# Kernel tuning notes

Measured on AMD Instinct MI355X. Metric: run time of the kernel, lower is better.

Reference implementation:

```python
import jax, jax.numpy as jnp
import numpy as np

T = 48        # target_size
B = 128       # batch of sequences (vmapped version of the per-sequence module)
S = 512       # seq_len
START = 46    # start_index
END = 47      # end_index
MIN = 0.0001  # self.minimum


def setup_inputs() -> dict:
    key = jax.random.key(0)
    k1, k2 = jax.random.split(key)
    features = jax.random.normal(k1, (B, S, T), dtype=jnp.float32)
    # __init_transition__: uniform matrix with start column / end row zeroed,
    # then MIN placed at those zeroed positions.
    u = jax.random.uniform(k2, (T, T), dtype=jnp.float32)
    start_mask = 1.0 - jax.nn.one_hot(jnp.full((T,), START), T)          # zeros column START
    end_mask = 1.0 - jax.nn.one_hot(jnp.full((T,), END), T).T            # zeros row END
    value = (1.0 - start_mask * end_mask) * MIN                          # MIN where masked out
    transition = u * start_mask * end_mask + value
    return {"features": features, "transition": transition}


def reference(features, transition):
    # CRF forward (partition-function) score, faithful to forward_score(),
    # batched over B sequences. features: [B, S, T], transition: [T, T].
    fv0 = MIN * (1.0 - jax.nn.one_hot(START, T, dtype=jnp.float32))      # [T]
    fv0 = jnp.broadcast_to(fv0, (B, T))

    def step(fv, feat_t):
        # score[b, i, j] = fv[b, j] + transition[i, j] + feat_t[b, i]
        score = fv[:, None, :] + transition[None, :, :] + feat_t[:, :, None]  # [B, T, T]
        # Faithful replication of the source's log_sum_exp: the max subtracted
        # inside exp is the per-row max indexed by j (column position), while the
        # max added back is indexed by i.
        rowmax = jnp.max(score, axis=2)                                   # [B, T]
        new_fv = rowmax + jnp.log(jnp.sum(jnp.exp(score - rowmax[:, None, :]), axis=2))
        return new_fv, None

    feats_time_major = jnp.swapaxes(features, 0, 1)                       # [S, B, T]
    fv, _ = jax.lax.scan(step, fv0, feats_time_major)

    # Terminal transition to END, then a single-row logsumexp (standard here).
    sc = fv + transition[END][None, :]                                    # [B, T]
    m = jnp.max(sc, axis=1)                                               # [B]
    return m + jnp.log(jnp.sum(jnp.exp(sc - m[:, None]), axis=1))         # [B]
```

## Files before the change

### kernel.cpp

```cpp
#include <hip/hip_runtime.h>
#include <math.h>


#define TT 48
#define BB 128
#define SS 512
#define STARTI 46
#define ENDI 47
#define MINV 0.0001f
#define CHUNK 32
#define NCHUNK (SS / CHUNK)
#define GPT 6
#define LOG2E 1.44269504088896340736f
#define LN2   0.69314718055994530942f

#if __has_builtin(__builtin_amdgcn_exp2f)
#define EXP2F(x) __builtin_amdgcn_exp2f(x)
#else
#define EXP2F(x) exp2f(x)
#endif
#if __has_builtin(__builtin_amdgcn_logf)
#define LOG2F(x) __builtin_amdgcn_logf(x)
#else
#define LOG2F(x) log2f(x)
#endif

template <int CTRL>
__device__ __forceinline__ float qperm_f(float x) {
#if __has_builtin(__builtin_amdgcn_update_dpp)
    return __int_as_float(__builtin_amdgcn_update_dpp(
        0, __float_as_int(x), CTRL, 0xF, 0xF, true));
#elif __has_builtin(__builtin_amdgcn_mov_dpp)
    return __int_as_float(
        __builtin_amdgcn_mov_dpp(__float_as_int(x), CTRL, 0xF, 0xF, true));
#else
    return __shfl_xor(x, (CTRL == 0xB1) ? 1 : 2, 64);
#endif
}

#if __has_builtin(__builtin_amdgcn_global_load_lds)
#define HAVE_GLOAD 1
__device__ __forceinline__ void gload16(const float* g, float* l) {
    __builtin_amdgcn_global_load_lds(
        (const __attribute__((address_space(1))) void*)g,
        (__attribute__((address_space(3))) void*)l, 16, 0, 0);
}
#else
#define HAVE_GLOAD 0
#endif

__global__ __launch_bounds__(64, 1) void crf_forward_kernel(
    const float* __restrict__ feats,
    const float* __restrict__ trans,
    float* __restrict__ out)
{
    const int lane = threadIdx.x;
    const int i16  = lane >> 2;
    const int jsub = lane & 3;
    const int j0   = jsub * 12;
    const int b    = blockIdx.x;

    __shared__ __align__(16) float fvb[TT];
    __shared__ __align__(16) float hb[TT];
    __shared__ __align__(16) float featbuf[2][CHUNK * TT];

    float tr2[3][12], E[3][12];
#pragma unroll
    for (int r = 0; r < 3; ++r) {
#pragma unroll
        for (int q = 0; q < 3; ++q) {
            float4 v = *reinterpret_cast<const float4*>(
                trans + (i16 + 16 * r) * TT + j0 + 4 * q);
            tr2[r][4 * q + 0] = v.x * LOG2E; tr2[r][4 * q + 1] = v.y * LOG2E;
            tr2[r][4 * q + 2] = v.z * LOG2E; tr2[r][4 * q + 3] = v.w * LOG2E;
        }
#pragma unroll
        for (int q = 0; q < 12; ++q) E[r][q] = EXP2F(tr2[r][q]);
    }

    const float* fb = feats + (size_t)b * SS * TT;

#if HAVE_GLOAD
#pragma unroll
    for (int k = 0; k < GPT; ++k)
        gload16(fb + k * 256 + lane * 4, &featbuf[0][k * 256]);
#else
#pragma unroll
    for (int k = 0; k < GPT; ++k)
        *reinterpret_cast<float4*>(&featbuf[0][k * 256 + lane * 4]) =
            *reinterpret_cast<const float4*>(fb + k * 256 + lane * 4);
#endif

    if (lane < TT) fvb[lane] = (lane == STARTI) ? 0.0f : (MINV * LOG2E);
    float fvi[3];
#pragma unroll
    for (int r = 0; r < 3; ++r)
        fvi[r] = ((i16 + 16 * r) == STARTI) ? 0.0f : (MINV * LOG2E);

#if HAVE_GLOAD
    asm volatile("s_waitcnt vmcnt(0)" ::: "memory");
#endif

    for (int c = 0; c < NCHUNK; ++c) {
        const int buf = c & 1;
        const bool hp = (c + 1 < NCHUNK);
        if (hp) {
#if HAVE_GLOAD
#pragma unroll
            for (int k = 0; k < GPT; ++k)
                gload16(fb + (c + 1) * (CHUNK * TT) + k * 256 + lane * 4,
                        &featbuf[buf ^ 1][k * 256]);
#else
#pragma unroll
            for (int k = 0; k < GPT; ++k)
                *reinterpret_cast<float4*>(&featbuf[buf ^ 1][k * 256 + lane * 4]) =
                    *reinterpret_cast<const float4*>(
                        fb + (c + 1) * (CHUNK * TT) + k * 256 + lane * 4);
#endif
        }

        for (int sl = 0; sl < CHUNK; ++sl) {
            float feat2[3];
#pragma unroll
            for (int r = 0; r < 3; ++r)
                feat2[r] = featbuf[buf][sl * TT + i16 + 16 * r] * LOG2E;

            float4 v0 = *reinterpret_cast<const float4*>(&fvb[j0]);
            float4 v1 = *reinterpret_cast<const float4*>(&fvb[j0 + 4]);
            float4 v2 = *reinterpret_cast<const float4*>(&fvb[j0 + 8]);
            float fvs[12] = {v0.x, v0.y, v0.z, v0.w, v1.x, v1.y,
                             v1.z, v1.w, v2.x, v2.y, v2.z, v2.w};

            float hs[3], qv2[3];
#pragma unroll
            for (int r = 0; r < 3; ++r) {
                float a[12];
#pragma unroll
                for (int q = 0; q < 12; ++q) a[q] = fvs[q] + tr2[r][q];
                float m0 = fmaxf(fmaxf(a[0], a[1]),  a[2]);
                float m1 = fmaxf(fmaxf(a[3], a[4]),  a[5]);
                float m2 = fmaxf(fmaxf(a[6], a[7]),  a[8]);
                float m3 = fmaxf(fmaxf(a[9], a[10]), a[11]);
                float M2 = fmaxf(fmaxf(fmaxf(m0, m1), m2), m3);
                M2 = fmaxf(M2, qperm_f<0xB1>(M2));
                M2 = fmaxf(M2, qperm_f<0x4E>(M2));
                hs[r]  = EXP2F((fvi[r] - feat2[r]) - M2);
                qv2[r] = M2 + 2.0f * feat2[r];
            }
            if (jsub == 0) {
                hb[i16]      = hs[0];
                hb[i16 + 16] = hs[1];
                hb[i16 + 32] = hs[2];
            }
            float4 h0 = *reinterpret_cast<const float4*>(&hb[j0]);
            float4 h1 = *reinterpret_cast<const float4*>(&hb[j0 + 4]);
            float4 h2 = *reinterpret_cast<const float4*>(&hb[j0 + 8]);
            float hv[12] = {h0.x, h0.y, h0.z, h0.w, h1.x, h1.y,
                            h1.z, h1.w, h2.x, h2.y, h2.z, h2.w};

            float nfv[3];
#pragma unroll
            for (int r = 0; r < 3; ++r) {
                float d0 = E[r][0] * hv[0], d1 = E[r][1] * hv[1];
                float d2 = E[r][2] * hv[2], d3 = E[r][3] * hv[3];
                d0 = fmaf(E[r][4],  hv[4],  d0); d1 = fmaf(E[r][5],  hv[5],  d1);
                d2 = fmaf(E[r][6],  hv[6],  d2); d3 = fmaf(E[r][7],  hv[7],  d3);
                d0 = fmaf(E[r][8],  hv[8],  d0); d1 = fmaf(E[r][9],  hv[9],  d1);
                d2 = fmaf(E[r][10], hv[10], d2); d3 = fmaf(E[r][11], hv[11], d3);
                float dot = (d0 + d1) + (d2 + d3);
                dot += qperm_f<0xB1>(dot);
                dot += qperm_f<0x4E>(dot);
                nfv[r] = qv2[r] + LOG2F(dot);
                fvi[r] = nfv[r];
            }
            if (jsub == 0) {
                fvb[i16]      = nfv[0];
                fvb[i16 + 16] = nfv[1];
                fvb[i16 + 32] = nfv[2];
            }
#if HAVE_GLOAD
            if (sl == CHUNK - 2 && hp)
                asm volatile("s_waitcnt vmcnt(0)" ::: "memory");
#endif
        }
    }

    {
        const float* te = trans + ENDI * TT;
        float sc[TT];
#pragma unroll
        for (int q = 0; q < 12; ++q) {
            float4 fv4 = *reinterpret_cast<const float4*>(&fvb[4 * q]);
            float4 te4 = *reinterpret_cast<const float4*>(te + 4 * q);
            sc[4 * q + 0] = fmaf(fv4.x, LN2, te4.x);
            sc[4 * q + 1] = fmaf(fv4.y, LN2, te4.y);
            sc[4 * q + 2] = fmaf(fv4.z, LN2, te4.z);
            sc[4 * q + 3] = fmaf(fv4.w, LN2, te4.w);
        }
        float m = sc[0];
#pragma unroll
        for (int j = 1; j < TT; ++j) m = fmaxf(m, sc[j]);
        float s = 0.0f;
#pragma unroll
        for (int j = 0; j < TT; ++j) s += __expf(sc[j] - m);
        if (lane == 0) out[b] = m + __logf(s);
    }
}

extern "C" void kernel_launch(void* const* d_in, const int* in_sizes, int n_in,
                              void* d_out, int out_size, void* d_ws, size_t ws_size,
                              hipStream_t stream) {
    (void)in_sizes; (void)n_in; (void)out_size; (void)d_ws; (void)ws_size;
    const float* feats = (const float*)d_in[0];
    const float* trans = (const float*)d_in[1];
    float* out = (float*)d_out;
    crf_forward_kernel<<<dim3(BB), dim3(64), 0, stream>>>(feats, trans, out);
}
```

Before: 258.2 us.

## Interleave two independent sequences per wavefront to hide serial-step latency

```diff
diff --git a/kernel.cpp b/kernel.cpp
--- a/kernel.cpp
+++ b/kernel.cpp
@@ -8,6 +8,8 @@
 #define STARTI 46
 #define ENDI 47
 #define MINV 0.0001f
+#define KSEQ 2
+#define NBLK (BB / KSEQ)
 #define CHUNK 32
 #define NCHUNK (SS / CHUNK)
 #define GPT 6
@@ -58,11 +60,11 @@
     const int i16  = lane >> 2;
     const int jsub = lane & 3;
     const int j0   = jsub * 12;
-    const int b    = blockIdx.x;
-
-    __shared__ __align__(16) float fvb[TT];
-    __shared__ __align__(16) float hb[TT];
-    __shared__ __align__(16) float featbuf[2][CHUNK * TT];
+    const int b0   = blockIdx.x * KSEQ;
+
+    __shared__ __align__(16) float fvb[KSEQ][TT];
+    __shared__ __align__(16) float hb[KSEQ][TT];
+    __shared__ __align__(16) float featbuf[KSEQ][2][CHUNK * TT];
 
     float tr2[3][12], E[3][12];
 #pragma unroll
@@ -78,24 +80,36 @@
         for (int q = 0; q < 12; ++q) E[r][q] = EXP2F(tr2[r][q]);
     }
 
-    const float* fb = feats + (size_t)b * SS * TT;
-
-#if HAVE_GLOAD
-#pragma unroll
-    for (int k = 0; k < GPT; ++k)
-        gload16(fb + k * 256 + lane * 4, &featbuf[0][k * 256]);
-#else
-#pragma unroll
-    for (int k = 0; k < GPT; ++k)
-        *reinterpret_cast<float4*>(&featbuf[0][k * 256 + lane * 4]) =
-            *reinterpret_cast<const float4*>(fb + k * 256 + lane * 4);
-#endif
-
-    if (lane < TT) fvb[lane] = (lane == STARTI) ? 0.0f : (MINV * LOG2E);
-    float fvi[3];
-#pragma unroll
-    for (int r = 0; r < 3; ++r)
-        fvi[r] = ((i16 + 16 * r) == STARTI) ? 0.0f : (MINV * LOG2E);
+    const float* fbs[KSEQ];
+#pragma unroll
+    for (int s = 0; s < KSEQ; ++s)
+        fbs[s] = feats + (size_t)(b0 + s) * SS * TT;
+
+#pragma unroll
+    for (int s = 0; s < KSEQ; ++s) {
+#if HAVE_GLOAD
+#pragma unroll
+        for (int k = 0; k < GPT; ++k)
+            gload16(fbs[s] + k * 256 + lane * 4, &featbuf[s][0][k * 256]);
+#else
+#pragma unroll
+        for (int k = 0; k < GPT; ++k)
+            *reinterpret_cast<float4*>(&featbuf[s][0][k * 256 + lane * 4]) =
+                *reinterpret_cast<const float4*>(fbs[s] + k * 256 + lane * 4);
+#endif
+    }
+
+    if (lane < TT) {
+#pragma unroll
+        for (int s = 0; s < KSEQ; ++s)
+            fvb[s][lane] = (lane == STARTI) ? 0.0f : (MINV * LOG2E);
+    }
+    float fvi[KSEQ][3];
+#pragma unroll
+    for (int s = 0; s < KSEQ; ++s)
+#pragma unroll
+        for (int r = 0; r < 3; ++r)
+            fvi[s][r] = ((i16 + 16 * r) == STARTI) ? 0.0f : (MINV * LOG2E);
 
 #if HAVE_GLOAD
     asm volatile("s_waitcnt vmcnt(0)" ::: "memory");
@@ -105,78 +119,111 @@
         const int buf = c & 1;
         const bool hp = (c + 1 < NCHUNK);
         if (hp) {
-#if HAVE_GLOAD
-#pragma unroll
-            for (int k = 0; k < GPT; ++k)
-                gload16(fb + (c + 1) * (CHUNK * TT) + k * 256 + lane * 4,
-                        &featbuf[buf ^ 1][k * 256]);
-#else
-#pragma unroll
-            for (int k = 0; k < GPT; ++k)
-                *reinterpret_cast<float4*>(&featbuf[buf ^ 1][k * 256 + lane * 4]) =
-                    *reinterpret_cast<const float4*>(
-                        fb + (c + 1) * (CHUNK * TT) + k * 256 + lane * 4);
-#endif
+#pragma unroll
+            for (int s = 0; s < KSEQ; ++s) {
+#if HAVE_GLOAD
+#pragma unroll
+                for (int k = 0; k < GPT; ++k)
+                    gload16(fbs[s] + (c + 1) * (CHUNK * TT) + k * 256 + lane * 4,
+                            &featbuf[s][buf ^ 1][k * 256]);
+#else
+#pragma unroll
+                for (int k = 0; k < GPT; ++k)
+                    *reinterpret_cast<float4*>(
+                        &featbuf[s][buf ^ 1][k * 256 + lane * 4]) =
+                        *reinterpret_cast<const float4*>(
+                            fbs[s] + (c + 1) * (CHUNK * TT) + k * 256 + lane * 4);
+#endif
+            }
         }
 
         for (int sl = 0; sl < CHUNK; ++sl) {
-            float feat2[3];
-#pragma unroll
-            for (int r = 0; r < 3; ++r)
-                feat2[r] = featbuf[buf][sl * TT + i16 + 16 * r] * LOG2E;
-
-            float4 v0 = *reinterpret_cast<const float4*>(&fvb[j0]);
-            float4 v1 = *reinterpret_cast<const float4*>(&fvb[j0 + 4]);
-            float4 v2 = *reinterpret_cast<const float4*>(&fvb[j0 + 8]);
-            float fvs[12] = {v0.x, v0.y, v0.z, v0.w, v1.x, v1.y,
-                             v1.z, v1.w, v2.x, v2.y, v2.z, v2.w};
-
-            float hs[3], qv2[3];
-#pragma unroll
-            for (int r = 0; r < 3; ++r) {
-                float a[12];
-#pragma unroll
-                for (int q = 0; q < 12; ++q) a[q] = fvs[q] + tr2[r][q];
-                float m0 = fmaxf(fmaxf(a[0], a[1]),  a[2]);
-                float m1 = fmaxf(fmaxf(a[3], a[4]),  a[5]);
-                float m2 = fmaxf(fmaxf(a[6], a[7]),  a[8]);
-                float m3 = fmaxf(fmaxf(a[9], a[10]), a[11]);
-                float M2 = fmaxf(fmaxf(fmaxf(m0, m1), m2), m3);
-                M2 = fmaxf(M2, qperm_f<0xB1>(M2));
-                M2 = fmaxf(M2, qperm_f<0x4E>(M2));
-                hs[r]  = EXP2F((fvi[r] - feat2[r]) - M2);
-                qv2[r] = M2 + 2.0f * feat2[r];
+            float feat2[KSEQ][3];
+#pragma unroll
+            for (int s = 0; s < KSEQ; ++s)
+#pragma unroll
+                for (int r = 0; r < 3; ++r)
+                    feat2[s][r] =
+                        featbuf[s][buf][sl * TT + i16 + 16 * r] * LOG2E;
+
+            float fvs[KSEQ][12];
+#pragma unroll
+            for (int s = 0; s < KSEQ; ++s) {
+                float4 v0 = *reinterpret_cast<const float4*>(&fvb[s][j0]);
+                float4 v1 = *reinterpret_cast<const float4*>(&fvb[s][j0 + 4]);
+                float4 v2 = *reinterpret_cast<const float4*>(&fvb[s][j0 + 8]);
+                fvs[s][0] = v0.x; fvs[s][1] = v0.y; fvs[s][2]  = v0.z; fvs[s][3]  = v0.w;
+                fvs[s][4] = v1.x; fvs[s][5] = v1.y; fvs[s][6]  = v1.z; fvs[s][7]  = v1.w;
+                fvs[s][8] = v2.x; fvs[s][9] = v2.y; fvs[s][10] = v2.z; fvs[s][11] = v2.w;
+            }
+
+            float hs[KSEQ][3], qv2[KSEQ][3];
+#pragma unroll
+            for (int s = 0; s < KSEQ; ++s) {
+#pragma unroll
+                for (int r = 0; r < 3; ++r) {
+                    float a[12];
+#pragma unroll
+                    for (int q = 0; q < 12; ++q) a[q] = fvs[s][q] + tr2[r][q];
+                    float m0 = fmaxf(fmaxf(a[0], a[1]),  a[2]);
+                    float m1 = fmaxf(fmaxf(a[3], a[4]),  a[5]);
+                    float m2 = fmaxf(fmaxf(a[6], a[7]),  a[8]);
+                    float m3 = fmaxf(fmaxf(a[9], a[10]), a[11]);
+                    float M2 = fmaxf(fmaxf(fmaxf(m0, m1), m2), m3);
+                    M2 = fmaxf(M2, qperm_f<0xB1>(M2));
+                    M2 = fmaxf(M2, qperm_f<0x4E>(M2));
+                    hs[s][r]  = EXP2F((fvi[s][r] - feat2[s][r]) - M2);
+                    qv2[s][r] = M2 + 2.0f * feat2[s][r];
+                }
             }
             if (jsub == 0) {
-                hb[i16]      = hs[0];
-                hb[i16 + 16] = hs[1];
-                hb[i16 + 32] = hs[2];
-            }
-            float4 h0 = *reinterpret_cast<const float4*>(&hb[j0]);
-            float4 h1 = *reinterpret_cast<const float4*>(&hb[j0 + 4]);
-            float4 h2 = *reinterpret_cast<const float4*>(&hb[j0 + 8]);
-            float hv[12] = {h0.x, h0.y, h0.z, h0.w, h1.x, h1.y,
-                            h1.z, h1.w, h2.x, h2.y, h2.z, h2.w};
-
-            float nfv[3];
-#pragma unroll
-            for (int r = 0; r < 3; ++r) {
-                float d0 = E[r][0] * hv[0], d1 = E[r][1] * hv[1];
-                float d2 = E[r][2] * hv[2], d3 = E[r][3] * hv[3];
-                d0 = fmaf(E[r][4],  hv[4],  d0); d1 = fmaf(E[r][5],  hv[5],  d1);
-                d2 = fmaf(E[r][6],  hv[6],  d2); d3 = fmaf(E[r][7],  hv[7],  d3);
-                d0 = fmaf(E[r][8],  hv[8],  d0); d1 = fmaf(E[r][9],  hv[9],  d1);
-                d2 = fmaf(E[r][10], hv[10], d2); d3 = fmaf(E[r][11], hv[11], d3);
-                float dot = (d0 + d1) + (d2 + d3);
-                dot += qperm_f<0xB1>(dot);
-                dot += qperm_f<0x4E>(dot);
-                nfv[r] = qv2[r] + LOG2F(dot);
-                fvi[r] = nfv[r];
+#pragma unroll
+                for (int s = 0; s < KSEQ; ++s) {
+                    hb[s][i16]      = hs[s][0];
+                    hb[s][i16 + 16] = hs[s][1];
+                    hb[s][i16 + 32] = hs[s][2];
+                }
+            }
+            float hv[KSEQ][12];
+#pragma unroll
+            for (int s = 0; s < KSEQ; ++s) {
+                float4 h0 = *reinterpret_cast<const float4*>(&hb[s][j0]);
+                float4 h1 = *reinterpret_cast<const float4*>(&hb[s][j0 + 4]);
+                float4 h2 = *reinterpret_cast<const float4*>(&hb[s][j0 + 8]);
+                hv[s][0] = h0.x; hv[s][1] = h0.y; hv[s][2]  = h0.z; hv[s][3]  = h0.w;
+                hv[s][4] = h1.x; hv[s][5] = h1.y; hv[s][6]  = h1.z; hv[s][7]  = h1.w;
+                hv[s][8] = h2.x; hv[s][9] = h2.y; hv[s][10] = h2.z; hv[s][11] = h2.w;
+            }
+
+            float nfv[KSEQ][3];
+#pragma unroll
+            for (int s = 0; s < KSEQ; ++s) {
+#pragma unroll
+                for (int r = 0; r < 3; ++r) {
+                    float d0 = E[r][0] * hv[s][0], d1 = E[r][1] * hv[s][1];
+                    float d2 = E[r][2] * hv[s][2], d3 = E[r][3] * hv[s][3];
+                    d0 = fmaf(E[r][4],  hv[s][4],  d0);
+                    d1 = fmaf(E[r][5],  hv[s][5],  d1);
+                    d2 = fmaf(E[r][6],  hv[s][6],  d2);
+                    d3 = fmaf(E[r][7],  hv[s][7],  d3);
+                    d0 = fmaf(E[r][8],  hv[s][8],  d0);
+                    d1 = fmaf(E[r][9],  hv[s][9],  d1);
+                    d2 = fmaf(E[r][10], hv[s][10], d2);
+                    d3 = fmaf(E[r][11], hv[s][11], d3);
+                    float dot = (d0 + d1) + (d2 + d3);
+                    dot += qperm_f<0xB1>(dot);
+                    dot += qperm_f<0x4E>(dot);
+                    nfv[s][r] = qv2[s][r] + LOG2F(dot);
+                    fvi[s][r] = nfv[s][r];
+                }
             }
             if (jsub == 0) {
-                fvb[i16]      = nfv[0];
-                fvb[i16 + 16] = nfv[1];
-                fvb[i16 + 32] = nfv[2];
+#pragma unroll
+                for (int s = 0; s < KSEQ; ++s) {
+                    fvb[s][i16]      = nfv[s][0];
+                    fvb[s][i16 + 16] = nfv[s][1];
+                    fvb[s][i16 + 32] = nfv[s][2];
+                }
             }
 #if HAVE_GLOAD
             if (sl == CHUNK - 2 && hp)
@@ -187,23 +234,26 @@
 
     {
         const float* te = trans + ENDI * TT;
-        float sc[TT];
-#pragma unroll
-        for (int q = 0; q < 12; ++q) {
-            float4 fv4 = *reinterpret_cast<const float4*>(&fvb[4 * q]);
-            float4 te4 = *reinterpret_cast<const float4*>(te + 4 * q);
-            sc[4 * q + 0] = fmaf(fv4.x, LN2, te4.x);
-            sc[4 * q + 1] = fmaf(fv4.y, LN2, te4.y);
-            sc[4 * q + 2] = fmaf(fv4.z, LN2, te4.z);
-            sc[4 * q + 3] = fmaf(fv4.w, LN2, te4.w);
-        }
-        float m = sc[0];
-#pragma unroll
-        for (int j = 1; j < TT; ++j) m = fmaxf(m, sc[j]);
-        float s = 0.0f;
-#pragma unroll
-        for (int j = 0; j < TT; ++j) s += __expf(sc[j] - m);
-        if (lane == 0) out[b] = m + __logf(s);
+#pragma unroll
+        for (int s = 0; s < KSEQ; ++s) {
+            float sc[TT];
+#pragma unroll
+            for (int q = 0; q < 12; ++q) {
+                float4 fv4 = *reinterpret_cast<const float4*>(&fvb[s][4 * q]);
+                float4 te4 = *reinterpret_cast<const float4*>(te + 4 * q);
+                sc[4 * q + 0] = fmaf(fv4.x, LN2, te4.x);
+                sc[4 * q + 1] = fmaf(fv4.y, LN2, te4.y);
+                sc[4 * q + 2] = fmaf(fv4.z, LN2, te4.z);
+                sc[4 * q + 3] = fmaf(fv4.w, LN2, te4.w);
+            }
+            float m = sc[0];
+#pragma unroll
+            for (int j = 1; j < TT; ++j) m = fmaxf(m, sc[j]);
+            float sum = 0.0f;
+#pragma unroll
+            for (int j = 0; j < TT; ++j) sum += __expf(sc[j] - m);
+            if (lane == 0) out[b0 + s] = m + __logf(sum);
+        }
     }
 }
 
@@ -214,5 +264,5 @@
     const float* feats = (const float*)d_in[0];
     const float* trans = (const float*)d_in[1];
     float* out = (float*)d_out;
-    crf_forward_kernel<<<dim3(BB), dim3(64), 0, stream>>>(feats, trans, out);
-}
+    crf_forward_kernel<<<dim3(NBLK), dim3(64), 0, stream>>>(feats, trans, out);
+}
```

Measured after the change: 410.6 us. 1.59x slower.

## Assign one full row per lane instead of splitting rows across four lanes

Applied to the files above, without the earlier changes.

```diff
diff --git a/kernel.cpp b/kernel.cpp
--- a/kernel.cpp
+++ b/kernel.cpp
@@ -25,19 +25,6 @@
 #define LOG2F(x) log2f(x)
 #endif
 
-template <int CTRL>
-__device__ __forceinline__ float qperm_f(float x) {
-#if __has_builtin(__builtin_amdgcn_update_dpp)
-    return __int_as_float(__builtin_amdgcn_update_dpp(
-        0, __float_as_int(x), CTRL, 0xF, 0xF, true));
-#elif __has_builtin(__builtin_amdgcn_mov_dpp)
-    return __int_as_float(
-        __builtin_amdgcn_mov_dpp(__float_as_int(x), CTRL, 0xF, 0xF, true));
-#else
-    return __shfl_xor(x, (CTRL == 0xB1) ? 1 : 2, 64);
-#endif
-}
-
 #if __has_builtin(__builtin_amdgcn_global_load_lds)
 #define HAVE_GLOAD 1
 __device__ __forceinline__ void gload16(const float* g, float* l) {
@@ -49,34 +36,32 @@
 #define HAVE_GLOAD 0
 #endif
 
+__device__ __forceinline__ float m3(float a, float b, float c) {
+    return fmaxf(fmaxf(a, b), c);
+}
+
 __global__ __launch_bounds__(64, 1) void crf_forward_kernel(
     const float* __restrict__ feats,
     const float* __restrict__ trans,
     float* __restrict__ out)
 {
     const int lane = threadIdx.x;
-    const int i16  = lane >> 2;
-    const int jsub = lane & 3;
-    const int j0   = jsub * 12;
+    const int row  = (lane < TT) ? lane : TT - 1;
     const int b    = blockIdx.x;
 
-    __shared__ __align__(16) float fvb[TT];
-    __shared__ __align__(16) float hb[TT];
+    __shared__ __align__(16) float fvx[TT];
+    __shared__ __align__(16) float hx[TT];
     __shared__ __align__(16) float featbuf[2][CHUNK * TT];
 
-    float tr2[3][12], E[3][12];
+    float tr2r[TT], Er[TT];
 #pragma unroll
-    for (int r = 0; r < 3; ++r) {
+    for (int q = 0; q < 12; ++q) {
+        float4 v = *reinterpret_cast<const float4*>(trans + row * TT + 4 * q);
+        tr2r[4 * q + 0] = v.x * LOG2E; tr2r[4 * q + 1] = v.y * LOG2E;
+        tr2r[4 * q + 2] = v.z * LOG2E; tr2r[4 * q + 3] = v.w * LOG2E;
+    }
 #pragma unroll
-        for (int q = 0; q < 3; ++q) {
-            float4 v = *reinterpret_cast<const float4*>(
-                trans + (i16 + 16 * r) * TT + j0 + 4 * q);
-            tr2[r][4 * q + 0] = v.x * LOG2E; tr2[r][4 * q + 1] = v.y * LOG2E;
-            tr2[r][4 * q + 2] = v.z * LOG2E; tr2[r][4 * q + 3] = v.w * LOG2E;
-        }
-#pragma unroll
-        for (int q = 0; q < 12; ++q) E[r][q] = EXP2F(tr2[r][q]);
-    }
+    for (int k = 0; k < TT; ++k) Er[k] = EXP2F(tr2r[k]);
 
     const float* fb = feats + (size_t)b * SS * TT;
 
@@ -91,11 +76,8 @@
             *reinterpret_cast<const float4*>(fb + k * 256 + lane * 4);
 #endif
 
-    if (lane < TT) fvb[lane] = (lane == STARTI) ? 0.0f : (MINV * LOG2E);
-    float fvi[3];
-#pragma unroll
-    for (int r = 0; r < 3; ++r)
-        fvi[r] = ((i16 + 16 * r) == STARTI) ? 0.0f : (MINV * LOG2E);
+    if (lane < TT) fvx[lane] = (lane == STARTI) ? 0.0f : (MINV * LOG2E);
+    float fv2i = (row == STARTI) ? 0.0f : (MINV * LOG2E);
 
 #if HAVE_GLOAD
     asm volatile("s_waitcnt vmcnt(0)" ::: "memory");
@@ -120,64 +102,54 @@
         }
 
         for (int sl = 0; sl < CHUNK; ++sl) {
-            float feat2[3];
+            const float feat2 = featbuf[buf][sl * TT + row] * LOG2E;
+
+            float g[TT];
 #pragma unroll
-            for (int r = 0; r < 3; ++r)
-                feat2[r] = featbuf[buf][sl * TT + i16 + 16 * r] * LOG2E;
+            for (int q = 0; q < 12; ++q) {
+                float4 v = *reinterpret_cast<const float4*>(&fvx[4 * q]);
+                g[4 * q + 0] = v.x; g[4 * q + 1] = v.y;
+                g[4 * q + 2] = v.z; g[4 * q + 3] = v.w;
+            }
+            float a[TT];
+#pragma unroll
+            for (int k = 0; k < TT; ++k) a[k] = g[k] + tr2r[k];
+            float t16[16];
+#pragma unroll
+            for (int u = 0; u < 16; ++u)
+                t16[u] = m3(a[3 * u], a[3 * u + 1], a[3 * u + 2]);
+            float t6_0 = m3(t16[0],  t16[1],  t16[2]);
+            float t6_1 = m3(t16[3],  t16[4],  t16[5]);
+            float t6_2 = m3(t16[6],  t16[7],  t16[8]);
+            float t6_3 = m3(t16[9],  t16[10], t16[11]);
+            float t6_4 = m3(t16[12], t16[13], t16[14]);
+            float t6_5 = t16[15];
+            const float M2 = fmaxf(m3(t6_0, t6_1, t6_2), m3(t6_3, t6_4, t6_5));
 
-            float4 v0 = *reinterpret_cast<const float4*>(&fvb[j0]);
-            float4 v1 = *reinterpret_cast<const float4*>(&fvb[j0 + 4]);
-            float4 v2 = *reinterpret_cast<const float4*>(&fvb[j0 + 8]);
-            float fvs[12] = {v0.x, v0.y, v0.z, v0.w, v1.x, v1.y,
-                             v1.z, v1.w, v2.x, v2.y, v2.z, v2.w};
+            const float h   = EXP2F((fv2i - feat2) - M2);
+            const float qv2 = M2 + 2.0f * feat2;
+            if (lane < TT) hx[lane] = h;
 
-            float hs[3], qv2[3];
+            float hg[TT];
 #pragma unroll
-            for (int r = 0; r < 3; ++r) {
-                float a[12];
+            for (int q = 0; q < 12; ++q) {
+                float4 v = *reinterpret_cast<const float4*>(&hx[4 * q]);
+                hg[4 * q + 0] = v.x; hg[4 * q + 1] = v.y;
+                hg[4 * q + 2] = v.z; hg[4 * q + 3] = v.w;
+            }
+            float acc[8];
 #pragma unroll
-                for (int q = 0; q < 12; ++q) a[q] = fvs[q] + tr2[r][q];
-                float m0 = fmaxf(fmaxf(a[0], a[1]),  a[2]);
-                float m1 = fmaxf(fmaxf(a[3], a[4]),  a[5]);
-                float m2 = fmaxf(fmaxf(a[6], a[7]),  a[8]);
-                float m3 = fmaxf(fmaxf(a[9], a[10]), a[11]);
-                float M2 = fmaxf(fmaxf(fmaxf(m0, m1), m2), m3);
-                M2 = fmaxf(M2, qperm_f<0xB1>(M2));
-                M2 = fmaxf(M2, qperm_f<0x4E>(M2));
-                hs[r]  = EXP2F((fvi[r] - feat2[r]) - M2);
-                qv2[r] = M2 + 2.0f * feat2[r];
-            }
-            if (jsub == 0) {
-                hb[i16]      = hs[0];
-                hb[i16 + 16] = hs[1];
-                hb[i16 + 32] = hs[2];
-            }
-            float4 h0 = *reinterpret_cast<const float4*>(&hb[j0]);
-            float4 h1 = *reinterpret_cast<const float4*>(&hb[j0 + 4]);
-            float4 h2 = *reinterpret_cast<const float4*>(&hb[j0 + 8]);
-            float hv[12] = {h0.x, h0.y, h0.z, h0.w, h1.x, h1.y,
-                            h1.z, h1.w, h2.x, h2.y, h2.z, h2.w};
+            for (int u = 0; u < 8; ++u) acc[u] = Er[u] * hg[u];
+#pragma unroll
+            for (int k = 8; k < TT; ++k)
+                acc[k & 7] = fmaf(Er[k], hg[k], acc[k & 7]);
+            const float dot = ((acc[0] + acc[1]) + (acc[2] + acc[3]))
+                            + ((acc[4] + acc[5]) + (acc[6] + acc[7]));
 
-            float nfv[3];
-#pragma unroll
-            for (int r = 0; r < 3; ++r) {
-                float d0 = E[r][0] * hv[0], d1 = E[r][1] * hv[1];
-                float d2 = E[r][2] * hv[2], d3 = E[r][3] * hv[3];
-                d0 = fmaf(E[r][4],  hv[4],  d0); d1 = fmaf(E[r][5],  hv[5],  d1);
-                d2 = fmaf(E[r][6],  hv[6],  d2); d3 = fmaf(E[r][7],  hv[7],  d3);
-                d0 = fmaf(E[r][8],  hv[8],  d0); d1 = fmaf(E[r][9],  hv[9],  d1);
-                d2 = fmaf(E[r][10], hv[10], d2); d3 = fmaf(E[r][11], hv[11], d3);
-                float dot = (d0 + d1) + (d2 + d3);
-                dot += qperm_f<0xB1>(dot);
-                dot += qperm_f<0x4E>(dot);
-                nfv[r] = qv2[r] + LOG2F(dot);
-                fvi[r] = nfv[r];
-            }
-            if (jsub == 0) {
-                fvb[i16]      = nfv[0];
-                fvb[i16 + 16] = nfv[1];
-                fvb[i16 + 32] = nfv[2];
-            }
+            const float nfv = qv2 + LOG2F(dot);
+            fv2i = nfv;
+            if (lane < TT) fvx[lane] = nfv;
+
 #if HAVE_GLOAD
             if (sl == CHUNK - 2 && hp)
                 asm volatile("s_waitcnt vmcnt(0)" ::: "memory");
@@ -190,7 +162,7 @@
         float sc[TT];
 #pragma unroll
         for (int q = 0; q < 12; ++q) {
-            float4 fv4 = *reinterpret_cast<const float4*>(&fvb[4 * q]);
+            float4 fv4 = *reinterpret_cast<const float4*>(&fvx[4 * q]);
             float4 te4 = *reinterpret_cast<const float4*>(te + 4 * q);
             sc[4 * q + 0] = fmaf(fv4.x, LN2, te4.x);
             sc[4 * q + 1] = fmaf(fv4.y, LN2, te4.y);
```

After: 272.3 us. 1.05x slower.
